# Performance work log

Hardware: AMD Instinct MI355X
Metric: run time of the kernel (lower is better)

The kernel has to match this reference:

```python
import jax, jax.numpy as jnp
import numpy as np
import math

HIDDEN = 768
NUM_HEADS = 12
HEAD_DIM = HIDDEN // NUM_HEADS
EPS = 1e-05
MU_LEARNED = 0.0    # registered buffer init value (inference mode)
SIGMA_LEARNED = 1.0 # registered buffer init value (inference mode)
SCALES = (0.5, 1.0, 2.0)


def make_pe(n, d):
    # Sinusoidal positional encoding, identical to PositionalEncoding buffer.
    pos = np.arange(n, dtype=np.float32)[:, None]
    div = np.exp(np.arange(0, d, 2, dtype=np.float32) * (-math.log(10000.0) / d))
    pe = np.zeros((n, d), dtype=np.float32)
    pe[:, 0::2] = np.sin(pos * div)
    pe[:, 1::2] = np.cos(pos * div)
    return jnp.asarray(pe)


def setup_inputs() -> dict:
    key = jax.random.key(0)
    ks = jax.random.split(key, 12)
    B, C, Hh, Ww = 8, 256, 32, 32
    feat = jax.random.normal(ks[0], (B, C, Hh, Ww), jnp.float32)
    I = jax.random.uniform(ks[1], (B, 1, Hh, Ww), jnp.float32)
    sc_c = 1.0 / math.sqrt(C)
    sd = 1.0 / math.sqrt(HIDDEN)
    proj_w = jax.random.normal(ks[2], (C, HIDDEN), jnp.float32) * sc_c  # 1x1 conv as matmul
    proj_b = jnp.zeros((HIDDEN,), jnp.float32)
    wq = jax.random.normal(ks[3], (HIDDEN, HIDDEN), jnp.float32) * sd
    bq = jnp.zeros((HIDDEN,), jnp.float32)
    wk = jax.random.normal(ks[4], (HIDDEN, HIDDEN), jnp.float32) * sd
    bk = jnp.zeros((HIDDEN,), jnp.float32)
    wv = jax.random.normal(ks[5], (HIDDEN, HIDDEN), jnp.float32) * sd
    bv = jnp.zeros((HIDDEN,), jnp.float32)
    wo = jax.random.normal(ks[6], (HIDDEN, HIDDEN), jnp.float32) * sd
    bo = jnp.zeros((HIDDEN,), jnp.float32)
    lam = jnp.float32(0.5)
    return dict(feat=feat, I=I, proj_w=proj_w, proj_b=proj_b,
                wq=wq, bq=bq, wk=wk, bk=bk, wv=wv, bv=bv, wo=wo, bo=bo, lam=lam)


def reference(feat, I, proj_w, proj_b, wq, bq, wk, bk, wv, bv, wo, bo, lam):
    B, C, Hh, Ww = feat.shape
    N = Hh * Ww
    # HiddenFeatureProjection: 1x1 conv projection -> flatten -> tokens [B, N, D]
    tokens = jnp.einsum('bchw,cd->bhwd', feat, proj_w).reshape(B, N, HIDDEN) + proj_b
    tokens = tokens + make_pe(N, HIDDEN)[None]
    # GaussianWeightModule (inference path, learned buffers mu=0, sigma=1)
    G = sum(jnp.exp(-(I - MU_LEARNED) ** 2 / (2.0 * (k * SIGMA_LEARNED) ** 2 + EPS))
            for k in SCALES) / float(len(SCALES))  # [B,1,H,W]
    g = G.reshape(B, N)                              # H*W == N by construction
    bias = g[:, :, None] * g[:, None, :]             # [B, N, N] outer product
    # GaussianEnhancedAttention
    q = (tokens @ wq + bq).reshape(B, N, NUM_HEADS, HEAD_DIM).transpose(0, 2, 1, 3)
    k = (tokens @ wk + bk).reshape(B, N, NUM_HEADS, HEAD_DIM).transpose(0, 2, 1, 3)
    v = (tokens @ wv + bv).reshape(B, N, NUM_HEADS, HEAD_DIM).transpose(0, 2, 1, 3)
    scores = jnp.einsum('bhnd,bhmd->bhnm', q, k) / math.sqrt(HEAD_DIM)
    scores = scores + lam * bias[:, None, :, :]
    attn = jax.nn.softmax(scores, axis=-1)
    out = jnp.einsum('bhnm,bhmd->bhnd', attn, v).transpose(0, 2, 1, 3).reshape(B, N, HIDDEN)
    return out @ wo + bo
```

## Files before the change

kernel.cpp:

```cpp
#include <hip/hip_runtime.h>
#include <hip/hip_bf16.h>
#include <math.h>

#define HIDDEN 768
#define NHEADS 12
#define HDIM   64
#define NTOK   1024
#define BATCH  8
#define CIN    256
#define M_ALL  (BATCH * NTOK)
#define LSTR   72

typedef __hip_bfloat16 bf16;
typedef short frag8 __attribute__((ext_vector_type(8)));
typedef short s16x4 __attribute__((ext_vector_type(4)));
typedef unsigned int u32x2 __attribute__((ext_vector_type(2)));
typedef float f32x4 __attribute__((ext_vector_type(4)));

#define GL2LDS(gp, lp) \
    __builtin_amdgcn_global_load_lds((const __attribute__((address_space(1))) void*)(gp), \
                                     (__attribute__((address_space(3))) void*)(lp), 16, 0, 0)

__device__ __forceinline__ short f2bs(float x){
    union { bf16 h; short s; } u; u.h = __float2bfloat16(x); return u.s;
}

__device__ __forceinline__ float gaussw(float x){
    float x2 = x * x;
    return (__expf(-x2 / 0.50001f) + __expf(-x2 / 2.00001f) + __expf(-x2 / 8.00001f)) * (1.0f / 3.0f);
}

__global__ __launch_bounds__(256) void prep_all(
    const float* __restrict__ wq, const float* __restrict__ wk,
    const float* __restrict__ wv, const float* __restrict__ wo,
    const float* __restrict__ proj_w, const float* __restrict__ feat,
    short* __restrict__ wtqkv, short* __restrict__ wtp, short* __restrict__ featT)
{
    __shared__ short t[64][65];
    const int blk = blockIdx.x;
    const float* W; short* WT; int K, N, k0, n0;
    if (blk < 576) {
        int p = blk / 144, rem = blk % 144;
        const float* srcs[4] = {wq, wk, wv, wo};
        W = srcs[p]; WT = wtqkv + (size_t)p * HIDDEN * HIDDEN;
        K = HIDDEN; N = HIDDEN; k0 = (rem / 12) * 64; n0 = (rem % 12) * 64;
    } else if (blk < 624) {
        int rem = blk - 576;
        W = proj_w; WT = wtp;
        K = CIN; N = HIDDEN; k0 = (rem / 12) * 64; n0 = (rem % 12) * 64;
    } else {
        int rem = blk - 624;
        int b = rem / 64; rem %= 64;
        W = feat + (size_t)b * CIN * NTOK; WT = featT + (size_t)b * NTOK * CIN;
        K = CIN; N = NTOK; k0 = (rem / 16) * 64; n0 = (rem % 16) * 64;
    }
    const int tid = threadIdx.x;
    #pragma unroll
    for (int it = 0; it < 16; it++) {
        int e = tid + 256 * it;
        int kk = e / 64, nn = e % 64;
        t[kk][nn] = f2bs(W[(size_t)(k0 + kk) * N + n0 + nn]);
    }
    __syncthreads();
    #pragma unroll
    for (int it = 0; it < 16; it++) {
        int e = tid + 256 * it;
        int nn = e / 64, kk = e % 64;
        WT[(size_t)(n0 + nn) * K + k0 + kk] = t[kk][nn];
    }
}

__global__ __launch_bounds__(256) void transpose_v(
    const short* __restrict__ v, short* __restrict__ vT,
    const float* __restrict__ I, float* __restrict__ g)
{
    if (blockIdx.y == BATCH * NHEADS) {
        int idx = blockIdx.x * 512 + threadIdx.x * 2;
        g[idx]     = gaussw(I[idx]);
        g[idx + 1] = gaussw(I[idx + 1]);
        return;
    }
    __shared__ short t[64][65];
    const int nt = blockIdx.x;
    const int bh = blockIdx.y;
    const int b = bh / NHEADS, h = bh % NHEADS;
    const int tid = threadIdx.x;
    #pragma unroll
    for (int it = 0; it < 16; it++) {
        int e = tid + 256 * it;
        int rr = e / 64, cc = e % 64;
        t[rr][cc] = v[(size_t)(b * NTOK + nt * 64 + rr) * HIDDEN + h * HDIM + cc];
    }
    __syncthreads();
    #pragma unroll
    for (int it = 0; it < 16; it++) {
        int e = tid + 256 * it;
        int c2 = e / 64, r2 = e % 64;
        vT[((size_t)bh * HDIM + c2) * NTOK + nt * 64 + r2] = t[r2][c2];
    }
}

__global__ __launch_bounds__(256) void gemm_mfma128(
    const short* __restrict__ A, const short* __restrict__ WT0, long wt_z,
    const float* __restrict__ b0, const float* __restrict__ b1, const float* __restrict__ b2,
    short* o0, short* o1, short* o2, int K)
{
    __shared__ short Al[128 * 32];
    __shared__ short Bl[128 * 32];
    const int z = blockIdx.z;
    const short* WT  = WT0 + (size_t)z * wt_z;
    const float* bias = (z == 0) ? b0 : (z == 1) ? b1 : b2;
    short* outv       = (z == 0) ? o0 : (z == 1) ? o1 : o2;

    const int tid  = threadIdx.x;
    const int m0   = blockIdx.x * 128;
    const int n0   = blockIdx.y * 128;
    const int lane = tid & 63, wid = tid >> 6;
    const int wm   = (wid >> 1) * 64, wn = (wid & 1) * 64;
    const int l16  = lane & 15, quad = lane >> 4;

    const int sr  = lane >> 2;
    const int ssg = (lane & 3) ^ ((sr >> 1) & 3);
    const int fsw = (l16 >> 1) & 3;

    const f32x4 z4 = {0.f, 0.f, 0.f, 0.f};
    f32x4 acc[4][4];
    #pragma unroll
    for (int i = 0; i < 4; i++)
        #pragma unroll
        for (int j = 0; j < 4; j++) acc[i][j] = z4;

    for (int k0 = 0; k0 < K; k0 += 32) {
        #pragma unroll
        for (int t = 0; t < 2; t++) {
            int rbase = wid * 32 + t * 16;
            int r = rbase + sr;
            GL2LDS(A  + (size_t)(m0 + r) * K + k0 + ssg * 8, &Al[rbase * 32]);
            GL2LDS(WT + (size_t)(n0 + r) * K + k0 + ssg * 8, &Bl[rbase * 32]);
        }
        __syncthreads();
        frag8 af[4], bfr[4];
        #pragma unroll
        for (int i = 0; i < 4; i++)
            af[i]  = *(const frag8*)&Al[(wm + i * 16 + l16) * 32 + ((quad ^ fsw) * 8)];
        #pragma unroll
        for (int j = 0; j < 4; j++)
            bfr[j] = *(const frag8*)&Bl[(wn + j * 16 + l16) * 32 + ((quad ^ fsw) * 8)];
        #pragma unroll
        for (int i = 0; i < 4; i++)
            #pragma unroll
            for (int j = 0; j < 4; j++)
                acc[i][j] = __builtin_amdgcn_mfma_f32_16x16x32_bf16(af[i], bfr[j], acc[i][j], 0, 0, 0);
        __syncthreads();
    }

    #pragma unroll
    for (int i = 0; i < 4; i++) {
        #pragma unroll
        for (int r = 0; r < 4; r++) {
            int m = m0 + wm + i * 16 + quad * 4 + r;
            #pragma unroll
            for (int j = 0; j < 4; j++) {
                int col = n0 + wn + j * 16 + l16;
                outv[(size_t)m * HIDDEN + col] = f2bs(acc[i][j][r] + bias[col]);
            }
        }
    }
}

template<int MODE>
__global__ __launch_bounds__(256) void gemm_mfma64(
    const short* __restrict__ A, const short* __restrict__ WT,
    const float* __restrict__ bias, void* outv, int K)
{
    __shared__ short Al[64 * 32];
    __shared__ short Bl[128 * 32];
    const int tid  = threadIdx.x;
    const int m0   = blockIdx.x * 64;
    const int n0   = blockIdx.y * 128;
    const int lane = tid & 63, wid = tid >> 6;
    const int wn   = wid * 32;
    const int l16  = lane & 15, quad = lane >> 4;

    const int sr  = lane >> 2;
    const int ssg = (lane & 3) ^ ((sr >> 1) & 3);
    const int fsw = (l16 >> 1) & 3;

    const f32x4 z4 = {0.f, 0.f, 0.f, 0.f};
    f32x4 acc[4][2];
    #pragma unroll
    for (int i = 0; i < 4; i++)
        #pragma unroll
        for (int j = 0; j < 2; j++) acc[i][j] = z4;

    for (int k0 = 0; k0 < K; k0 += 32) {
        GL2LDS(A + (size_t)(m0 + wid * 16 + sr) * K + k0 + ssg * 8, &Al[(wid * 16) * 32]);
        #pragma unroll
        for (int t = 0; t < 2; t++) {
            int rbase = wid * 32 + t * 16;
            GL2LDS(WT + (size_t)(n0 + rbase + sr) * K + k0 + ssg * 8, &Bl[rbase * 32]);
        }
        __syncthreads();
        frag8 af[4], bfr[2];
        #pragma unroll
        for (int i = 0; i < 4; i++)
            af[i]  = *(const frag8*)&Al[(i * 16 + l16) * 32 + ((quad ^ fsw) * 8)];
        #pragma unroll
        for (int j = 0; j < 2; j++)
            bfr[j] = *(const frag8*)&Bl[(wn + j * 16 + l16) * 32 + ((quad ^ fsw) * 8)];
        #pragma unroll
        for (int i = 0; i < 4; i++)
            #pragma unroll
            for (int j = 0; j < 2; j++)
                acc[i][j] = __builtin_amdgcn_mfma_f32_16x16x32_bf16(af[i], bfr[j], acc[i][j], 0, 0, 0);
        __syncthreads();
    }

    const float kfac = -9.210340371976184f / 768.0f;
    #pragma unroll
    for (int i = 0; i < 4; i++) {
        #pragma unroll
        for (int r = 0; r < 4; r++) {
            int m = m0 + i * 16 + quad * 4 + r;
            #pragma unroll
            for (int j = 0; j < 2; j++) {
                int col = n0 + wn + j * 16 + l16;
                float val = acc[i][j][r] + bias[col];
                if (MODE == 1) {
                    int n_tok = m & (NTOK - 1);
                    float ang = (float)n_tok * expf((float)(2 * (col >> 1)) * kfac);
                    val += (col & 1) ? cosf(ang) : sinf(ang);
                }
                if (MODE == 2) ((float*)outv)[(size_t)m * HIDDEN + col] = val;
                else           ((short*)outv)[(size_t)m * HIDDEN + col] = f2bs(val);
            }
        }
    }
}

__global__ __launch_bounds__(256, 3) void attn_mfma(
    const short* __restrict__ q, const short* __restrict__ k, const short* __restrict__ vT,
    const float* __restrict__ g, const float* __restrict__ lam_p, short* __restrict__ out)
{
    __shared__ short Pl[128 * LSTR];
    __shared__ short Ks[2][64 * 64];
    __shared__ short Vt[2][64 * 64];

    const int tid  = threadIdx.x;
    const int lin  = blockIdx.x;
    const int xcd  = lin & 7, slot = lin >> 3;
    const int b    = xcd;
    const int h    = slot >> 3;
    const int qt   = slot & 7;
    const float L2E  = 1.4426950408889634f;
    const float lam2 = lam_p[0] * L2E;
    const float scl  = 0.125f * L2E;
    const int lane = tid & 63, wave = tid >> 6;
    const int l16  = lane & 15, quad = lane >> 4;

    const int sr   = lane >> 3;
    const int slin = lane & 7;
    const int ssg  = slin ^ sr;
    const int fsw  = l16 & 7;

    const size_t kb  = (size_t)b * NTOK * HIDDEN + h * HDIM;
    const size_t vtb = (size_t)(b * NHEADS + h) * HDIM * NTOK;
    const float* gk  = g + b * NTOK;

    frag8 aq[2][2];
    #pragma unroll
    for (int half = 0; half < 2; half++)
        #pragma unroll
        for (int kc = 0; kc < 2; kc++)
            aq[half][kc] = *(const frag8*)&q[(size_t)(b * NTOK + qt * 128 + wave * 32 + half * 16 + l16) * HIDDEN
                                             + h * HDIM + kc * 32 + quad * 8];
    float gq[2];
    #pragma unroll
    for (int half = 0; half < 2; half++)
        gq[half] = lam2 * gk[qt * 128 + wave * 32 + half * 16 + l16];

    #pragma unroll
    for (int t = 0; t < 2; t++) {
        int rbase = wave * 16 + t * 8;
        int r = rbase + sr;
        GL2LDS(k  + kb  + (size_t)r * HIDDEN + ssg * 8,  &Ks[0][rbase * 64]);
        GL2LDS(vT + vtb + (size_t)r * NTOK + ssg * 8,    &Vt[0][rbase * 64]);
    }
    __syncthreads();

    const f32x4 z4 = {0.f, 0.f, 0.f, 0.f};
    f32x4 o_acc[2][4];
    #pragma unroll
    for (int half = 0; half < 2; half++)
        #pragma unroll
        for (int d = 0; d < 4; d++) o_acc[half][d] = z4;
    float l_run[2] = {0.f, 0.f};

    for (int jt = 0; jt < 16; jt++) {
        const int cur = jt & 1;
        f32x4 gk4[4];
        #pragma unroll
        for (int t4 = 0; t4 < 4; t4++)
            gk4[t4] = *(const f32x4*)&gk[jt * 64 + t4 * 16 + quad * 4];
        __builtin_amdgcn_sched_barrier(0);
        if (jt < 15) {
            #pragma unroll
            for (int t = 0; t < 2; t++) {
                int rbase = wave * 16 + t * 8;
                int r = rbase + sr;
                GL2LDS(k  + kb  + (size_t)((jt + 1) * 64 + r) * HIDDEN + ssg * 8, &Ks[cur ^ 1][rbase * 64]);
                GL2LDS(vT + vtb + (size_t)r * NTOK + (jt + 1) * 64 + ssg * 8,     &Vt[cur ^ 1][rbase * 64]);
            }
        }

        float p[2][4][4];
        #pragma unroll
        for (int t4 = 0; t4 < 4; t4++) {
            frag8 ak0 = *(const frag8*)&Ks[cur][(t4 * 16 + l16) * 64 + ((quad ^ fsw) * 8)];
            frag8 ak1 = *(const frag8*)&Ks[cur][(t4 * 16 + l16) * 64 + (((quad + 4) ^ fsw) * 8)];
            #pragma unroll
            for (int half = 0; half < 2; half++) {
                f32x4 a = z4;
                a = __builtin_amdgcn_mfma_f32_16x16x32_bf16(ak0, aq[half][0], a, 0, 0, 0);
                a = __builtin_amdgcn_mfma_f32_16x16x32_bf16(ak1, aq[half][1], a, 0, 0, 0);
                #pragma unroll
                for (int r = 0; r < 4; r++) p[half][t4][r] = a[r];
            }
        }

        #pragma unroll
        for (int half = 0; half < 2; half++)
            #pragma unroll
            for (int t4 = 0; t4 < 4; t4++) {
                float e0 = exp2f(fmaf(p[half][t4][0], scl, gq[half] * gk4[t4][0]));
                float e1 = exp2f(fmaf(p[half][t4][1], scl, gq[half] * gk4[t4][1]));
                float e2 = exp2f(fmaf(p[half][t4][2], scl, gq[half] * gk4[t4][2]));
                float e3 = exp2f(fmaf(p[half][t4][3], scl, gq[half] * gk4[t4][3]));
                l_run[half] += (e0 + e1) + (e2 + e3);
                unsigned lo, hi;
                asm("v_cvt_pk_bf16_f32 %0, %1, %2" : "=v"(lo) : "v"(e0), "v"(e1));
                asm("v_cvt_pk_bf16_f32 %0, %1, %2" : "=v"(hi) : "v"(e2), "v"(e3));
                u32x2 w = {lo, hi};
                *(u32x2*)&Pl[(wave * 32 + half * 16 + l16) * LSTR + t4 * 16 + quad * 4] = w;
            }

        frag8 ap[2][2];
        #pragma unroll
        for (int half = 0; half < 2; half++)
            #pragma unroll
            for (int kc = 0; kc < 2; kc++)
                ap[half][kc] = *(const frag8*)&Pl[(wave * 32 + half * 16 + l16) * LSTR + kc * 32 + quad * 8];
        #pragma unroll
        for (int d = 0; d < 4; d++) {
            frag8 av0 = *(const frag8*)&Vt[cur][(d * 16 + l16) * 64 + ((quad ^ fsw) * 8)];
            frag8 av1 = *(const frag8*)&Vt[cur][(d * 16 + l16) * 64 + (((quad + 4) ^ fsw) * 8)];
            #pragma unroll
            for (int half = 0; half < 2; half++) {
                o_acc[half][d] = __builtin_amdgcn_mfma_f32_16x16x32_bf16(ap[half][0], av0, o_acc[half][d], 0, 0, 0);
                o_acc[half][d] = __builtin_amdgcn_mfma_f32_16x16x32_bf16(ap[half][1], av1, o_acc[half][d], 0, 0, 0);
            }
        }
        __syncthreads();
    }

    #pragma unroll
    for (int half = 0; half < 2; half++) {
        float l = l_run[half];
        l += __shfl_xor(l, 16);
        l += __shfl_xor(l, 32);
        #pragma unroll
        for (int r = 0; r < 4; r++) {
            float lq = __shfl(l, (lane & 48) | (quad * 4 + r));
            float inv_l = 1.0f / lq;
            int row = qt * 128 + wave * 32 + half * 16 + quad * 4 + r;
            #pragma unroll
            for (int d = 0; d < 4; d++)
                out[(size_t)(b * NTOK + row) * HIDDEN + h * HDIM + d * 16 + l16]
                    = f2bs(o_acc[half][d][r] * inv_l);
        }
    }
}

extern "C" void kernel_launch(void* const* d_in, const int* in_sizes, int n_in,
                              void* d_out, int out_size, void* d_ws, size_t ws_size,
                              hipStream_t stream)
{
    const float* feat   = (const float*)d_in[0];
    const float* I      = (const float*)d_in[1];
    const float* proj_w = (const float*)d_in[2];
    const float* proj_b = (const float*)d_in[3];
    const float* wq     = (const float*)d_in[4];
    const float* bq     = (const float*)d_in[5];
    const float* wk     = (const float*)d_in[6];
    const float* bk     = (const float*)d_in[7];
    const float* wv     = (const float*)d_in[8];
    const float* bv     = (const float*)d_in[9];
    const float* wo     = (const float*)d_in[10];
    const float* bo     = (const float*)d_in[11];
    const float* lam    = (const float*)d_in[12];
    float* out = (float*)d_out;

    short* wtqkv = (short*)d_ws;
    short* wto   = wtqkv + (size_t)3 * HIDDEN * HIDDEN;
    short* wtp   = wto   + (size_t)HIDDEN * HIDDEN;
    short* tokens= wtp   + (size_t)HIDDEN * CIN;
    short* qbuf  = tokens+ (size_t)M_ALL * HIDDEN;
    short* featT = qbuf;
    short* vTb   = tokens;
    short* kbuf  = (short*)d_out;
    short* vbuf  = kbuf + (size_t)M_ALL * HIDDEN;
    float* gbuf  = (float*)wtp;

    prep_all<<<1136, 256, 0, stream>>>(wq, wk, wv, wo, proj_w, feat, wtqkv, wtp, featT);
    gemm_mfma64<1><<<dim3(128, 6), 256, 0, stream>>>(featT, wtp, proj_b, tokens, CIN);
    gemm_mfma128<<<dim3(64, 6, 3), 256, 0, stream>>>(tokens, wtqkv, (long)HIDDEN * HIDDEN,
                                                     bq, bk, bv,
                                                     qbuf, kbuf, vbuf, HIDDEN);
    transpose_v<<<dim3(16, 97), 256, 0, stream>>>(vbuf, vTb, I, gbuf);
    attn_mfma<<<768, 256, 0, stream>>>(qbuf, kbuf, vTb, gbuf, lam, qbuf);
    gemm_mfma64<2><<<dim3(128, 6), 256, 0, stream>>>(qbuf, wto, bo, out, HIDDEN);
}
```

Measured before the change: 230.5 us.

## Load V fragments directly to registers, stage gaussian weights in LDS, raise occupancy

Drops the double-buffered V tile from shared memory. Each wave now loads its V^T fragments straight from global memory into registers at the top of every key tile. The per-batch gaussian weight vector is staged once into LDS instead of being re-read from global each iteration. Launch bounds go from 3 to 4 blocks per CU, using the LDS freed by removing the V tile. This trades LDS traffic and footprint for redundant global/L2 reads of V across the four waves, and for more register pressure from the prefetched V fragments.

```diff
diff --git a/kernel.cpp b/kernel.cpp
--- a/kernel.cpp
+++ b/kernel.cpp
@@ -238,13 +238,13 @@
     }
 }
 
-__global__ __launch_bounds__(256, 3) void attn_mfma(
+__global__ __launch_bounds__(256, 4) void attn_mfma(
     const short* __restrict__ q, const short* __restrict__ k, const short* __restrict__ vT,
     const float* __restrict__ g, const float* __restrict__ lam_p, short* __restrict__ out)
 {
     __shared__ short Pl[128 * LSTR];
     __shared__ short Ks[2][64 * 64];
-    __shared__ short Vt[2][64 * 64];
+    __shared__ float gLs[NTOK];
 
     const int tid  = threadIdx.x;
     const int lin  = blockIdx.x;
@@ -265,7 +265,8 @@
 
     const size_t kb  = (size_t)b * NTOK * HIDDEN + h * HDIM;
     const size_t vtb = (size_t)(b * NHEADS + h) * HDIM * NTOK;
-    const float* gk  = g + b * NTOK;
+
+    for (int i = tid; i < NTOK; i += 256) gLs[i] = g[b * NTOK + i];
 
     frag8 aq[2][2];
     #pragma unroll
@@ -274,19 +275,19 @@
         for (int kc = 0; kc < 2; kc++)
             aq[half][kc] = *(const frag8*)&q[(size_t)(b * NTOK + qt * 128 + wave * 32 + half * 16 + l16) * HIDDEN
                                              + h * HDIM + kc * 32 + quad * 8];
-    float gq[2];
-    #pragma unroll
-    for (int half = 0; half < 2; half++)
-        gq[half] = lam2 * gk[qt * 128 + wave * 32 + half * 16 + l16];
 
     #pragma unroll
     for (int t = 0; t < 2; t++) {
         int rbase = wave * 16 + t * 8;
         int r = rbase + sr;
-        GL2LDS(k  + kb  + (size_t)r * HIDDEN + ssg * 8,  &Ks[0][rbase * 64]);
-        GL2LDS(vT + vtb + (size_t)r * NTOK + ssg * 8,    &Vt[0][rbase * 64]);
+        GL2LDS(k + kb + (size_t)r * HIDDEN + ssg * 8, &Ks[0][rbase * 64]);
     }
     __syncthreads();
+
+    float gq[2];
+    #pragma unroll
+    for (int half = 0; half < 2; half++)
+        gq[half] = lam2 * gLs[qt * 128 + wave * 32 + half * 16 + l16];
 
     const f32x4 z4 = {0.f, 0.f, 0.f, 0.f};
     f32x4 o_acc[2][4];
@@ -298,18 +299,19 @@
 
     for (int jt = 0; jt < 16; jt++) {
         const int cur = jt & 1;
-        f32x4 gk4[4];
-        #pragma unroll
-        for (int t4 = 0; t4 < 4; t4++)
-            gk4[t4] = *(const f32x4*)&gk[jt * 64 + t4 * 16 + quad * 4];
+        frag8 av[4][2];
+        #pragma unroll
+        for (int d = 0; d < 4; d++) {
+            av[d][0] = *(const frag8*)&vT[vtb + (size_t)(d * 16 + l16) * NTOK + jt * 64 + quad * 8];
+            av[d][1] = *(const frag8*)&vT[vtb + (size_t)(d * 16 + l16) * NTOK + jt * 64 + 32 + quad * 8];
+        }
         __builtin_amdgcn_sched_barrier(0);
         if (jt < 15) {
             #pragma unroll
             for (int t = 0; t < 2; t++) {
                 int rbase = wave * 16 + t * 8;
                 int r = rbase + sr;
-                GL2LDS(k  + kb  + (size_t)((jt + 1) * 64 + r) * HIDDEN + ssg * 8, &Ks[cur ^ 1][rbase * 64]);
-                GL2LDS(vT + vtb + (size_t)r * NTOK + (jt + 1) * 64 + ssg * 8,     &Vt[cur ^ 1][rbase * 64]);
+                GL2LDS(k + kb + (size_t)((jt + 1) * 64 + r) * HIDDEN + ssg * 8, &Ks[cur ^ 1][rbase * 64]);
             }
         }
 
@@ -329,13 +331,14 @@
         }
 
         #pragma unroll
-        for (int half = 0; half < 2; half++)
-            #pragma unroll
-            for (int t4 = 0; t4 < 4; t4++) {
-                float e0 = exp2f(fmaf(p[half][t4][0], scl, gq[half] * gk4[t4][0]));
-                float e1 = exp2f(fmaf(p[half][t4][1], scl, gq[half] * gk4[t4][1]));
-                float e2 = exp2f(fmaf(p[half][t4][2], scl, gq[half] * gk4[t4][2]));
-                float e3 = exp2f(fmaf(p[half][t4][3], scl, gq[half] * gk4[t4][3]));
+        for (int t4 = 0; t4 < 4; t4++) {
+            f32x4 gk4 = *(const f32x4*)&gLs[jt * 64 + t4 * 16 + quad * 4];
+            #pragma unroll
+            for (int half = 0; half < 2; half++) {
+                float e0 = exp2f(fmaf(p[half][t4][0], scl, gq[half] * gk4[0]));
+                float e1 = exp2f(fmaf(p[half][t4][1], scl, gq[half] * gk4[1]));
+                float e2 = exp2f(fmaf(p[half][t4][2], scl, gq[half] * gk4[2]));
+                float e3 = exp2f(fmaf(p[half][t4][3], scl, gq[half] * gk4[3]));
                 l_run[half] += (e0 + e1) + (e2 + e3);
                 unsigned lo, hi;
                 asm("v_cvt_pk_bf16_f32 %0, %1, %2" : "=v"(lo) : "v"(e0), "v"(e1));
@@ -343,6 +346,7 @@
                 u32x2 w = {lo, hi};
                 *(u32x2*)&Pl[(wave * 32 + half * 16 + l16) * LSTR + t4 * 16 + quad * 4] = w;
             }
+        }
 
         frag8 ap[2][2];
         #pragma unroll
@@ -352,12 +356,10 @@
                 ap[half][kc] = *(const frag8*)&Pl[(wave * 32 + half * 16 + l16) * LSTR + kc * 32 + quad * 8];
         #pragma unroll
         for (int d = 0; d < 4; d++) {
-            frag8 av0 = *(const frag8*)&Vt[cur][(d * 16 + l16) * 64 + ((quad ^ fsw) * 8)];
-            frag8 av1 = *(const frag8*)&Vt[cur][(d * 16 + l16) * 64 + (((quad + 4) ^ fsw) * 8)];
             #pragma unroll
             for (int half = 0; half < 2; half++) {
-                o_acc[half][d] = __builtin_amdgcn_mfma_f32_16x16x32_bf16(ap[half][0], av0, o_acc[half][d], 0, 0, 0);
-                o_acc[half][d] = __builtin_amdgcn_mfma_f32_16x16x32_bf16(ap[half][1], av1, o_acc[half][d], 0, 0, 0);
+                o_acc[half][d] = __builtin_amdgcn_mfma_f32_16x16x32_bf16(ap[half][0], av[d][0], o_acc[half][d], 0, 0, 0);
+                o_acc[half][d] = __builtin_amdgcn_mfma_f32_16x16x32_bf16(ap[half][1], av[d][1], o_acc[half][d], 0, 0, 0);
             }
         }
         __syncthreads();
```

Result: slower. 265.2 us (+15.0%).
